# Kernel optimization log

Measured on AMD Instinct MI355X. Metric: run time of the kernel, lower is better.

The kernel has to match this reference:

```python
import jax, jax.numpy as jnp
import numpy as np
import math

E = 8          # num_experts
IN = 1024      # input_size
HID = 512      # head_size (expert hidden)
TOP_K = 2
B, P = 8, 1024


def setup_inputs() -> dict:
    key = jax.random.key(0)
    k1, k2, k3, k4, k5 = jax.random.split(key, 5)
    # expert weights init like ParallelExperts.reset_parameters (uniform xavier-ish)
    std1 = math.sqrt(2.0 / (IN + HID)); a1 = math.sqrt(3.0) * std1
    std2 = math.sqrt(2.0 / (HID + IN)); a2 = math.sqrt(3.0) * std2
    return {
        "x": jax.random.normal(k1, (B, P, IN), dtype=jnp.float32),
        "Q_isp": jax.random.normal(k2, (B, P, 1, IN), dtype=jnp.float32),
        "K_isp": jax.random.normal(k3, (B, P, E, IN), dtype=jnp.float32),
        "w1": jax.random.uniform(k4, (E, IN, HID), minval=-a1, maxval=a1, dtype=jnp.float32),
        "w2": jax.random.uniform(k5, (E, HID, IN), minval=-a2, maxval=a2, dtype=jnp.float32),
    }


def _gates(Q_isp, K_isp):
    # attention-based gating, eval path (no noise)
    N = K_isp.shape[2]
    scale = 1.0 / math.sqrt(K_isp.shape[-1])
    # [B,P,1,N] -> [T,N]
    scores = jnp.einsum('bpqd,bpnd->bpqn', Q_isp, K_isp)[:, :, 0, :].reshape(-1, N) * scale
    logits = jnp.nan_to_num(scores, nan=0.0, posinf=20.0, neginf=-20.0)
    probs = jax.nn.softmax(logits, axis=1)
    top_g, top_i = jax.lax.top_k(probs, TOP_K)
    # renormalize top-k gates; denominator detached as in torch (.detach())
    top_g = top_g / jax.lax.stop_gradient(top_g.sum(axis=1, keepdims=True) + 1e-6)
    T = probs.shape[0]
    gates = jnp.zeros_like(probs).at[jnp.arange(T)[:, None], top_i].set(top_g)
    return gates  # [T, E]


def reference(x, Q_isp, K_isp, w1, w2):
    gates = _gates(Q_isp, K_isp)                       # [T,E]
    T = gates.shape[0]
    xt = x.reshape(T, -1)                              # [T,IN]
    # grouped expert GEMMs (dense-masked form; gates are 0 off top-k)
    h = jax.nn.gelu(jnp.einsum('ti,eio->teo', xt, w1), approximate=False)  # [T,E,HID]
    y = jnp.einsum('teo,eoi->tei', h, w2)              # [T,E,IN]
    out = jnp.einsum('tei,te->ti', y, gates)           # combine with gates
    return out.reshape(x.shape)
```

## Files before the change

### kernel.cpp

```cpp
#include <hip/hip_runtime.h>
#include <math.h>

#define TT 8192
#define NE 8
#define DIN 1024
#define DH 512
#define MT_MAX 136

typedef __attribute__((ext_vector_type(8))) short short8;
typedef __attribute__((ext_vector_type(4))) float f32x4;
typedef __attribute__((ext_vector_type(4))) unsigned short us4;

static const size_t NSLOT      = (size_t)(2 * TT + NE * 128);
static const size_t OFF_BASE   = 0;
static const size_t OFF_TOKEXP = 256;
static const size_t OFF_GPAIR  = OFF_TOKEXP + (size_t)TT * 8;
static const size_t OFF_SLOT0  = OFF_GPAIR  + (size_t)TT * 8;
static const size_t OFF_SLOT1  = OFF_SLOT0  + (size_t)TT * 4;
static const size_t OFF_TOK    = OFF_SLOT1  + (size_t)TT * 4;
static const size_t OFF_GATE   = OFF_TOK    + NSLOT * 4;
static const size_t OFF_XB     = OFF_GATE   + NSLOT * 4;
static const size_t OFF_W1T    = OFF_XB     + (size_t)TT * DIN * 2;
static const size_t OFF_W2T    = OFF_W1T    + (size_t)NE * DH * DIN * 2;
static const size_t OFF_H      = OFF_W2T    + (size_t)NE * DIN * DH * 2;
static const size_t OFF_Y      = OFF_H      + NSLOT * DH * 2;

__device__ __forceinline__ unsigned short f2bf(float f) {
    union { float f; unsigned u; } v; v.f = f;
    unsigned r = (v.u + 0x7fffu + ((v.u >> 16) & 1u)) >> 16;
    return (unsigned short)r;
}
__device__ __forceinline__ float bf2f(unsigned short u) {
    union { unsigned u; float f; } v; v.u = ((unsigned)u) << 16;
    return v.f;
}
__device__ __forceinline__ void async_copy16(const void* g, void* l) {
    __builtin_amdgcn_global_load_lds(
        (const __attribute__((address_space(1))) void*)g,
        (__attribute__((address_space(3))) void*)l, 16, 0, 0);
}

__device__ __forceinline__ float gelu_erf(float u) {
    float z  = 0.70710678118f * u;
    float az = fabsf(z);
    float t  = __builtin_amdgcn_rcpf(__builtin_fmaf(0.3275911f, az, 1.0f));
    float p  = t * (0.254829592f + t * (-0.284496736f + t * (1.421413741f +
               t * (-1.453152027f + t * 1.061405429f))));
    float e2 = exp2f(-1.4426950408889634f * az * az);
    float er = __builtin_fmaf(-p, e2, 1.0f);
    er = copysignf(er, z);
    return 0.5f * u * (1.0f + er);
}

__global__ __launch_bounds__(256) void prep_kernel(
    const float* __restrict__ x, const float* __restrict__ w1, const float* __restrict__ w2,
    const float* __restrict__ Q, const float* __restrict__ Kc,
    unsigned short* __restrict__ xb, unsigned short* __restrict__ w1t,
    unsigned short* __restrict__ w2t,
    int2* __restrict__ tokexp, float2* __restrict__ gpair)
{
    __shared__ float tile[32][33];
    int bid = blockIdx.x;
    int tid = threadIdx.x;

    if (bid < 2048) {
        int wave = tid >> 6, lane = tid & 63;
        int t = bid * 4 + wave;
        const float4* q4 = reinterpret_cast<const float4*>(Q + (size_t)t * DIN);
        const float4* k4 = reinterpret_cast<const float4*>(Kc + (size_t)t * NE * DIN);
        float4 q[4];
#pragma unroll
        for (int j = 0; j < 4; ++j) q[j] = q4[j * 64 + lane];
        float part[NE];
#pragma unroll
        for (int e = 0; e < NE; ++e) {
            float s = 0.0f;
#pragma unroll
            for (int j = 0; j < 4; ++j) {
                float4 kv = k4[e * 256 + j * 64 + lane];
                s += q[j].x * kv.x + q[j].y * kv.y + q[j].z * kv.z + q[j].w * kv.w;
            }
            part[e] = s;
        }
#pragma unroll
        for (int e = 0; e < NE; ++e) {
#pragma unroll
            for (int m = 1; m < 64; m <<= 1) part[e] += __shfl_xor(part[e], m);
        }
        if (lane == 0) {
            float s[NE];
#pragma unroll
            for (int e = 0; e < NE; ++e) {
                float v = part[e] * 0.03125f;
                if (isnan(v)) v = 0.0f;
                else if (isinf(v)) v = (v > 0.0f) ? 20.0f : -20.0f;
                s[e] = v;
            }
            float m = s[0];
            for (int e = 1; e < NE; ++e) m = fmaxf(m, s[e]);
            float p[NE]; float sum = 0.0f;
            for (int e = 0; e < NE; ++e) { p[e] = expf(s[e] - m); sum += p[e]; }
            float inv = 1.0f / sum;
            for (int e = 0; e < NE; ++e) p[e] *= inv;
            int i0 = 0;
            for (int e = 1; e < NE; ++e) if (p[e] > p[i0]) i0 = e;
            int i1 = (i0 == 0) ? 1 : 0;
            for (int e = 0; e < NE; ++e) if (e != i0 && p[e] > p[i1]) i1 = e;
            float denom = p[i0] + p[i1] + 1e-6f;
            tokexp[t] = make_int2(i0, i1);
            gpair[t]  = make_float2(p[i0] / denom, p[i1] / denom);
        }
    } else if (bid < 6144) {
        size_t i = ((size_t)(bid - 2048) * 256 + tid) * 8;
        float4 a = *reinterpret_cast<const float4*>(x + i);
        float4 b = *reinterpret_cast<const float4*>(x + i + 4);
        us4 o0 = { f2bf(a.x), f2bf(a.y), f2bf(a.z), f2bf(a.w) };
        us4 o1 = { f2bf(b.x), f2bf(b.y), f2bf(b.z), f2bf(b.w) };
        *reinterpret_cast<us4*>(xb + i)     = o0;
        *reinterpret_cast<us4*>(xb + i + 4) = o1;
    } else {
        const float* src; unsigned short* dst; int K, N, e, k0, n0;
        if (bid < 10240) {
            int r = bid - 6144; e = r >> 9; int rem = r & 511;
            k0 = (rem & 31) * 32; n0 = (rem >> 5) * 32;
            src = w1; dst = w1t; K = DIN; N = DH;
        } else {
            int r = bid - 10240; e = r >> 9; int rem = r & 511;
            k0 = (rem & 15) * 32; n0 = (rem >> 4) * 32;
            src = w2; dst = w2t; K = DH; N = DIN;
        }
        int tx = tid & 31, ty = tid >> 5;
        const float* s = src + ((size_t)e * K + k0) * N + n0;
#pragma unroll
        for (int r2 = 0; r2 < 32; r2 += 8) tile[ty + r2][tx] = s[(size_t)(ty + r2) * N + tx];
        __syncthreads();
        unsigned short* d = dst + ((size_t)e * N + n0) * K + k0;
#pragma unroll
        for (int r2 = 0; r2 < 32; r2 += 8) d[(size_t)(ty + r2) * K + tx] = f2bf(tile[tx][ty + r2]);
    }
}

__global__ __launch_bounds__(1024) void route_kernel(
    const int2* __restrict__ tokexp, const float2* __restrict__ gpair,
    int* __restrict__ base,
    int* __restrict__ tok_list, float* __restrict__ gate_list,
    int* __restrict__ slot0, int* __restrict__ slot1)
{
    int e = blockIdx.x;
    int tid = threadIdx.x;
    int wave = tid >> 6, lane = tid & 63;
    __shared__ int hist[NE];
    __shared__ int wsum[16];
    __shared__ int running;

    if (tid < NE) hist[tid] = 0;
    __syncthreads();

    int lc[NE];
#pragma unroll
    for (int j = 0; j < NE; ++j) lc[j] = 0;
#pragma unroll
    for (int r = 0; r < TT / 1024; ++r) {
        int2 te = tokexp[r * 1024 + tid];
#pragma unroll
        for (int j = 0; j < NE; ++j) lc[j] += (te.x == j ? 1 : 0) + (te.y == j ? 1 : 0);
    }
#pragma unroll
    for (int j = 0; j < NE; ++j) {
        int v = lc[j];
#pragma unroll
        for (int m = 1; m < 64; m <<= 1) v += __shfl_xor(v, m);
        if (lane == 0) atomicAdd(&hist[j], v);
    }
    __syncthreads();

    int basep[NE + 1];
    basep[0] = 0;
#pragma unroll
    for (int j = 0; j < NE; ++j) basep[j + 1] = basep[j] + ((hist[j] + 127) & ~127);

    if (tid == 0) {
        base[e] = basep[e];
        if (e == 0) base[NE] = basep[NE];
        running = basep[e];
    }
    __syncthreads();

    int myb = basep[e];
    int cnt_e = hist[e];
#pragma unroll 1
    for (int r = 0; r < TT / 1024; ++r) {
        int t = r * 1024 + tid;
        int2 te = tokexp[t];
        float2 g = gpair[t];
        bool f0 = (te.x == e), f1 = (te.y == e);
        bool f = f0 || f1;
        unsigned long long mask = __ballot(f);
        int mypos = __popcll(mask & ((1ull << lane) - 1ull));
        if (lane == 0) wsum[wave] = __popcll(mask);
        __syncthreads();
        int off = 0, total = 0;
        for (int w = 0; w < 16; ++w) {
            int c = wsum[w];
            if (w < wave) off += c;
            total += c;
        }
        int pos = running + off + mypos;
        if (f) {
            tok_list[pos]  = t;
            gate_list[pos] = f0 ? g.x : g.y;
            if (f0) slot0[t] = pos; else slot1[t] = pos;
        }
        __syncthreads();
        if (tid == 0) running += total;
        __syncthreads();
    }

    int padn = ((cnt_e + 127) & ~127) - cnt_e;
    if (tid < padn) {
        tok_list[myb + cnt_e + tid]  = 0;
        gate_list[myb + cnt_e + tid] = 0.0f;
    }
}

__global__ __launch_bounds__(256) void gemm1_kernel(
    const unsigned short* __restrict__ xb, const unsigned short* __restrict__ w1t,
    const int* __restrict__ base,
    const int* __restrict__ tok_list, unsigned short* __restrict__ h)
{
    int bv[NE + 1];
#pragma unroll
    for (int i = 0; i <= NE; ++i) bv[i] = base[i];
    int g0 = blockIdx.x * 128;
    if (g0 >= bv[NE]) return;
    int e = 0;
#pragma unroll
    for (int i = 1; i < NE; ++i) if (g0 >= bv[i]) e = i;

    int n0 = blockIdx.y * 128;

    __shared__ __align__(16) char smem[65536];

    int tid = threadIdx.x;
    int w = tid >> 6, lane = tid & 63;
    int wm = w & 1, wn = w >> 1;
    int mcol = lane & 15;
    int kq = (lane >> 4) * 8;

    int ra0 = tok_list[g0 + (2 * w + 0) * 16 + mcol];
    int ra1 = tok_list[g0 + (2 * w + 1) * 16 + mcol];

    const unsigned short* w1e = w1t + (size_t)e * DH * DIN;
    const unsigned short* pa0 = xb + (size_t)ra0 * DIN + kq;
    const unsigned short* pa1 = xb + (size_t)ra1 * DIN + kq;
    const unsigned short* pb0 = w1e + (size_t)(n0 + (2 * w + 0) * 16 + mcol) * DIN + kq;
    const unsigned short* pb1 = w1e + (size_t)(n0 + (2 * w + 1) * 16 + mcol) * DIN + kq;

    int d0 = (2 * w + 0) * 1024;
    int d1 = (2 * w + 1) * 1024;

#define STAGE1(buf, koff) do { \
    async_copy16(pa0 + (koff),      (buf) + d0); \
    async_copy16(pa1 + (koff),      (buf) + d1); \
    async_copy16(pa0 + (koff) + 32, (buf) + 8192  + d0); \
    async_copy16(pa1 + (koff) + 32, (buf) + 8192  + d1); \
    async_copy16(pb0 + (koff),      (buf) + 16384 + d0); \
    async_copy16(pb1 + (koff),      (buf) + 16384 + d1); \
    async_copy16(pb0 + (koff) + 32, (buf) + 24576 + d0); \
    async_copy16(pb1 + (koff) + 32, (buf) + 24576 + d1); \
} while (0)

    f32x4 acc[4][4];
#pragma unroll
    for (int i = 0; i < 4; i++)
#pragma unroll
        for (int j = 0; j < 4; j++) acc[i][j] = {0.f, 0.f, 0.f, 0.f};

    char* cur = smem;
    char* nxt = smem + 32768;

    STAGE1(cur, 0);
    __syncthreads();

    const int NT = DIN / 64;
    for (int t = 0; t < NT; ++t) {
        if (t + 1 < NT) STAGE1(nxt, (t + 1) * 64);
#pragma unroll
        for (int half = 0; half < 2; ++half) {
            const char* cb = cur + half * 8192;
            short8 af[4], bfr[4];
#pragma unroll
            for (int mt = 0; mt < 4; ++mt)
                af[mt] = *reinterpret_cast<const short8*>(cb + (wm * 4 + mt) * 1024 + lane * 16);
#pragma unroll
            for (int nt = 0; nt < 4; ++nt)
                bfr[nt] = *reinterpret_cast<const short8*>(cb + 16384 + (wn * 4 + nt) * 1024 + lane * 16);
#pragma unroll
            for (int mt = 0; mt < 4; ++mt)
#pragma unroll
                for (int nt = 0; nt < 4; ++nt)
                    acc[mt][nt] = __builtin_amdgcn_mfma_f32_16x16x32_bf16(af[mt], bfr[nt], acc[mt][nt], 0, 0, 0);
        }
        __syncthreads();
        char* tmp = cur; cur = nxt; nxt = tmp;
    }
#undef STAGE1

#pragma unroll
    for (int mt = 0; mt < 4; ++mt) {
        int rbase = (wm * 4 + mt) * 16 + ((lane >> 4) * 4);
#pragma unroll
        for (int r = 0; r < 4; ++r) {
            int row = rbase + r;
#pragma unroll
            for (int nt = 0; nt < 4; ++nt) {
                float g = gelu_erf(acc[mt][nt][r]);
                int col = n0 + (wn * 4 + nt) * 16 + mcol;
                h[(size_t)(g0 + row) * DH + col] = f2bf(g);
            }
        }
    }
}

__global__ __launch_bounds__(256) void gemm2_kernel(
    const unsigned short* __restrict__ h, const unsigned short* __restrict__ w2t,
    const int* __restrict__ base,
    const float* __restrict__ gate_list, unsigned short* __restrict__ y)
{
    int bv[NE + 1];
#pragma unroll
    for (int i = 0; i <= NE; ++i) bv[i] = base[i];
    int g0 = blockIdx.x * 128;
    if (g0 >= bv[NE]) return;
    int e = 0;
#pragma unroll
    for (int i = 1; i < NE; ++i) if (g0 >= bv[i]) e = i;

    int n0 = blockIdx.y * 128;

    __shared__ __align__(16) char smem[65536];

    int tid = threadIdx.x;
    int w = tid >> 6, lane = tid & 63;
    int wm = w & 1, wn = w >> 1;
    int mcol = lane & 15;
    int kq = (lane >> 4) * 8;

    const unsigned short* w2e = w2t + (size_t)e * DIN * DH;
    const unsigned short* pa0 = h + (size_t)(g0 + (2 * w + 0) * 16 + mcol) * DH + kq;
    const unsigned short* pa1 = h + (size_t)(g0 + (2 * w + 1) * 16 + mcol) * DH + kq;
    const unsigned short* pb0 = w2e + (size_t)(n0 + (2 * w + 0) * 16 + mcol) * DH + kq;
    const unsigned short* pb1 = w2e + (size_t)(n0 + (2 * w + 1) * 16 + mcol) * DH + kq;

    int d0 = (2 * w + 0) * 1024;
    int d1 = (2 * w + 1) * 1024;

#define STAGE2(buf, koff) do { \
    async_copy16(pa0 + (koff),      (buf) + d0); \
    async_copy16(pa1 + (koff),      (buf) + d1); \
    async_copy16(pa0 + (koff) + 32, (buf) + 8192  + d0); \
    async_copy16(pa1 + (koff) + 32, (buf) + 8192  + d1); \
    async_copy16(pb0 + (koff),      (buf) + 16384 + d0); \
    async_copy16(pb1 + (koff),      (buf) + 16384 + d1); \
    async_copy16(pb0 + (koff) + 32, (buf) + 24576 + d0); \
    async_copy16(pb1 + (koff) + 32, (buf) + 24576 + d1); \
} while (0)

    f32x4 acc[4][4];
#pragma unroll
    for (int i = 0; i < 4; i++)
#pragma unroll
        for (int j = 0; j < 4; j++) acc[i][j] = {0.f, 0.f, 0.f, 0.f};

    char* cur = smem;
    char* nxt = smem + 32768;

    STAGE2(cur, 0);
    __syncthreads();

    const int NT = DH / 64;
    for (int t = 0; t < NT; ++t) {
        if (t + 1 < NT) STAGE2(nxt, (t + 1) * 64);
#pragma unroll
        for (int half = 0; half < 2; ++half) {
            const char* cb = cur + half * 8192;
            short8 af[4], bfr[4];
#pragma unroll
            for (int mt = 0; mt < 4; ++mt)
                af[mt] = *reinterpret_cast<const short8*>(cb + (wm * 4 + mt) * 1024 + lane * 16);
#pragma unroll
            for (int nt = 0; nt < 4; ++nt)
                bfr[nt] = *reinterpret_cast<const short8*>(cb + 16384 + (wn * 4 + nt) * 1024 + lane * 16);
#pragma unroll
            for (int mt = 0; mt < 4; ++mt)
#pragma unroll
                for (int nt = 0; nt < 4; ++nt)
                    acc[mt][nt] = __builtin_amdgcn_mfma_f32_16x16x32_bf16(af[mt], bfr[nt], acc[mt][nt], 0, 0, 0);
        }
        __syncthreads();
        char* tmp = cur; cur = nxt; nxt = tmp;
    }
#undef STAGE2

#pragma unroll
    for (int mt = 0; mt < 4; ++mt) {
        int rbase = (wm * 4 + mt) * 16 + ((lane >> 4) * 4);
#pragma unroll
        for (int r = 0; r < 4; ++r) {
            int row = rbase + r;
            float g = gate_list[g0 + row];
#pragma unroll
            for (int nt = 0; nt < 4; ++nt) {
                int col = n0 + (wn * 4 + nt) * 16 + mcol;
                y[(size_t)(g0 + row) * DIN + col] = f2bf(acc[mt][nt][r] * g);
            }
        }
    }
}

__global__ __launch_bounds__(256) void combine_kernel(
    const unsigned short* __restrict__ y,
    const int* __restrict__ slot0, const int* __restrict__ slot1,
    float* __restrict__ out)
{
    int c = threadIdx.x * 4;
#pragma unroll
    for (int r = 0; r < 4; ++r) {
        int t = blockIdx.x * 4 + r;
        const unsigned short* y0 = y + (size_t)slot0[t] * DIN + c;
        const unsigned short* y1 = y + (size_t)slot1[t] * DIN + c;
        us4 u0 = *reinterpret_cast<const us4*>(y0);
        us4 u1 = *reinterpret_cast<const us4*>(y1);
        float4 o;
        o.x = bf2f(u0.x) + bf2f(u1.x);
        o.y = bf2f(u0.y) + bf2f(u1.y);
        o.z = bf2f(u0.z) + bf2f(u1.z);
        o.w = bf2f(u0.w) + bf2f(u1.w);
        *reinterpret_cast<float4*>(out + (size_t)t * DIN + c) = o;
    }
}

extern "C" void kernel_launch(void* const* d_in, const int* in_sizes, int n_in,
                              void* d_out, int out_size, void* d_ws, size_t ws_size,
                              hipStream_t stream) {
    const float* x  = (const float*)d_in[0];
    const float* Q  = (const float*)d_in[1];
    const float* K  = (const float*)d_in[2];
    const float* w1 = (const float*)d_in[3];
    const float* w2 = (const float*)d_in[4];
    float* out = (float*)d_out;

    char* ws = (char*)d_ws;
    int*    base      = (int*)(ws + OFF_BASE);
    int2*   tokexp    = (int2*)(ws + OFF_TOKEXP);
    float2* gpair     = (float2*)(ws + OFF_GPAIR);
    int*    slot0     = (int*)(ws + OFF_SLOT0);
    int*    slot1     = (int*)(ws + OFF_SLOT1);
    int*    tok_list  = (int*)(ws + OFF_TOK);
    float*  gate_list = (float*)(ws + OFF_GATE);
    unsigned short* xb  = (unsigned short*)(ws + OFF_XB);
    unsigned short* w1t = (unsigned short*)(ws + OFF_W1T);
    unsigned short* w2t = (unsigned short*)(ws + OFF_W2T);
    unsigned short* h   = (unsigned short*)(ws + OFF_H);
    unsigned short* y   = (unsigned short*)(ws + OFF_Y);

    prep_kernel<<<14336, 256, 0, stream>>>(x, w1, w2, Q, K, xb, w1t, w2t, tokexp, gpair);
    route_kernel<<<NE, 1024, 0, stream>>>(tokexp, gpair, base, tok_list, gate_list, slot0, slot1);
    gemm1_kernel<<<dim3(MT_MAX, DH / 128), 256, 0, stream>>>(xb, w1t, base, tok_list, h);
    gemm2_kernel<<<dim3(MT_MAX, DIN / 128), 256, 0, stream>>>(h, w2t, base, gate_list, y);
    combine_kernel<<<TT / 4, 256, 0, stream>>>(y, slot0, slot1, out);
}
```

Baseline: 551.5 us.

## Replace double-buffered K loop with 4-slot, 3-deep async copy pipeline

Both expert GEMM kernels now stage K-slices of 32 instead of 64 into a four-slot LDS ring. Three stages are prefetched ahead, and the loop waits on exact vmcnt counts before a single barrier per iteration. The goal is to hide more global-load latency and drop the trailing per-iteration syncthreads. In exchange the kernels run twice as many loop iterations, and correctness now depends on the hand-counted vmcnt values matching the four copies issued per stage.

```diff
diff --git a/kernel.cpp b/kernel.cpp
--- a/kernel.cpp
+++ b/kernel.cpp
@@ -260,14 +260,10 @@
     int d1 = (2 * w + 1) * 1024;
 
 #define STAGE1(buf, koff) do { \
-    async_copy16(pa0 + (koff),      (buf) + d0); \
-    async_copy16(pa1 + (koff),      (buf) + d1); \
-    async_copy16(pa0 + (koff) + 32, (buf) + 8192  + d0); \
-    async_copy16(pa1 + (koff) + 32, (buf) + 8192  + d1); \
-    async_copy16(pb0 + (koff),      (buf) + 16384 + d0); \
-    async_copy16(pb1 + (koff),      (buf) + 16384 + d1); \
-    async_copy16(pb0 + (koff) + 32, (buf) + 24576 + d0); \
-    async_copy16(pb1 + (koff) + 32, (buf) + 24576 + d1); \
+    async_copy16(pa0 + (koff), (buf) + d0); \
+    async_copy16(pa1 + (koff), (buf) + d1); \
+    async_copy16(pb0 + (koff), (buf) + 8192 + d0); \
+    async_copy16(pb1 + (koff), (buf) + 8192 + d1); \
 } while (0)
 
     f32x4 acc[4][4];
@@ -276,33 +272,34 @@
 #pragma unroll
         for (int j = 0; j < 4; j++) acc[i][j] = {0.f, 0.f, 0.f, 0.f};
 
-    char* cur = smem;
-    char* nxt = smem + 32768;
-
-    STAGE1(cur, 0);
-    __syncthreads();
-
-    const int NT = DIN / 64;
+    STAGE1(smem + 0 * 16384, 0);
+    STAGE1(smem + 1 * 16384, 32);
+    STAGE1(smem + 2 * 16384, 64);
+
+    const int NT = DIN / 32;
     for (int t = 0; t < NT; ++t) {
-        if (t + 1 < NT) STAGE1(nxt, (t + 1) * 64);
-#pragma unroll
-        for (int half = 0; half < 2; ++half) {
-            const char* cb = cur + half * 8192;
-            short8 af[4], bfr[4];
-#pragma unroll
-            for (int mt = 0; mt < 4; ++mt)
-                af[mt] = *reinterpret_cast<const short8*>(cb + (wm * 4 + mt) * 1024 + lane * 16);
+        if (t < NT - 2)       asm volatile("s_waitcnt vmcnt(8)" ::: "memory");
+        else if (t == NT - 2) asm volatile("s_waitcnt vmcnt(4)" ::: "memory");
+        else                  asm volatile("s_waitcnt vmcnt(0)" ::: "memory");
+        __builtin_amdgcn_sched_barrier(0);
+        __builtin_amdgcn_s_barrier();
+        __builtin_amdgcn_sched_barrier(0);
+        if (t + 3 < NT) STAGE1(smem + ((t + 3) & 3) * 16384, (t + 3) * 32);
+
+        const char* cb = smem + (t & 3) * 16384;
+        short8 af[4], bfr[4];
+#pragma unroll
+        for (int mt = 0; mt < 4; ++mt)
+            af[mt] = *reinterpret_cast<const short8*>(cb + (wm * 4 + mt) * 1024 + lane * 16);
+#pragma unroll
+        for (int nt = 0; nt < 4; ++nt)
+            bfr[nt] = *reinterpret_cast<const short8*>(cb + 8192 + (wn * 4 + nt) * 1024 + lane * 16);
+#pragma unroll
+        for (int mt = 0; mt < 4; ++mt)
 #pragma unroll
             for (int nt = 0; nt < 4; ++nt)
-                bfr[nt] = *reinterpret_cast<const short8*>(cb + 16384 + (wn * 4 + nt) * 1024 + lane * 16);
-#pragma unroll
-            for (int mt = 0; mt < 4; ++mt)
-#pragma unroll
-                for (int nt = 0; nt < 4; ++nt)
-                    acc[mt][nt] = __builtin_amdgcn_mfma_f32_16x16x32_bf16(af[mt], bfr[nt], acc[mt][nt], 0, 0, 0);
-        }
-        __syncthreads();
-        char* tmp = cur; cur = nxt; nxt = tmp;
+                acc[mt][nt] = __builtin_amdgcn_mfma_f32_16x16x32_bf16(af[mt], bfr[nt], acc[mt][nt], 0, 0, 0);
+        __builtin_amdgcn_sched_barrier(0);
     }
 #undef STAGE1
 
@@ -356,14 +353,10 @@
     int d1 = (2 * w + 1) * 1024;
 
 #define STAGE2(buf, koff) do { \
-    async_copy16(pa0 + (koff),      (buf) + d0); \
-    async_copy16(pa1 + (koff),      (buf) + d1); \
-    async_copy16(pa0 + (koff) + 32, (buf) + 8192  + d0); \
-    async_copy16(pa1 + (koff) + 32, (buf) + 8192  + d1); \
-    async_copy16(pb0 + (koff),      (buf) + 16384 + d0); \
-    async_copy16(pb1 + (koff),      (buf) + 16384 + d1); \
-    async_copy16(pb0 + (koff) + 32, (buf) + 24576 + d0); \
-    async_copy16(pb1 + (koff) + 32, (buf) + 24576 + d1); \
+    async_copy16(pa0 + (koff), (buf) + d0); \
+    async_copy16(pa1 + (koff), (buf) + d1); \
+    async_copy16(pb0 + (koff), (buf) + 8192 + d0); \
+    async_copy16(pb1 + (koff), (buf) + 8192 + d1); \
 } while (0)
 
     f32x4 acc[4][4];
@@ -372,33 +365,34 @@
 #pragma unroll
         for (int j = 0; j < 4; j++) acc[i][j] = {0.f, 0.f, 0.f, 0.f};
 
-    char* cur = smem;
-    char* nxt = smem + 32768;
-
-    STAGE2(cur, 0);
-    __syncthreads();
-
-    const int NT = DH / 64;
+    STAGE2(smem + 0 * 16384, 0);
+    STAGE2(smem + 1 * 16384, 32);
+    STAGE2(smem + 2 * 16384, 64);
+
+    const int NT = DH / 32;
     for (int t = 0; t < NT; ++t) {
-        if (t + 1 < NT) STAGE2(nxt, (t + 1) * 64);
-#pragma unroll
-        for (int half = 0; half < 2; ++half) {
-            const char* cb = cur + half * 8192;
-            short8 af[4], bfr[4];
-#pragma unroll
-            for (int mt = 0; mt < 4; ++mt)
-                af[mt] = *reinterpret_cast<const short8*>(cb + (wm * 4 + mt) * 1024 + lane * 16);
+        if (t < NT - 2)       asm volatile("s_waitcnt vmcnt(8)" ::: "memory");
+        else if (t == NT - 2) asm volatile("s_waitcnt vmcnt(4)" ::: "memory");
+        else                  asm volatile("s_waitcnt vmcnt(0)" ::: "memory");
+        __builtin_amdgcn_sched_barrier(0);
+        __builtin_amdgcn_s_barrier();
+        __builtin_amdgcn_sched_barrier(0);
+        if (t + 3 < NT) STAGE2(smem + ((t + 3) & 3) * 16384, (t + 3) * 32);
+
+        const char* cb = smem + (t & 3) * 16384;
+        short8 af[4], bfr[4];
+#pragma unroll
+        for (int mt = 0; mt < 4; ++mt)
+            af[mt] = *reinterpret_cast<const short8*>(cb + (wm * 4 + mt) * 1024 + lane * 16);
+#pragma unroll
+        for (int nt = 0; nt < 4; ++nt)
+            bfr[nt] = *reinterpret_cast<const short8*>(cb + 8192 + (wn * 4 + nt) * 1024 + lane * 16);
+#pragma unroll
+        for (int mt = 0; mt < 4; ++mt)
 #pragma unroll
             for (int nt = 0; nt < 4; ++nt)
-                bfr[nt] = *reinterpret_cast<const short8*>(cb + 16384 + (wn * 4 + nt) * 1024 + lane * 16);
-#pragma unroll
-            for (int mt = 0; mt < 4; ++mt)
-#pragma unroll
-                for (int nt = 0; nt < 4; ++nt)
-                    acc[mt][nt] = __builtin_amdgcn_mfma_f32_16x16x32_bf16(af[mt], bfr[nt], acc[mt][nt], 0, 0, 0);
-        }
-        __syncthreads();
-        char* tmp = cur; cur = nxt; nxt = tmp;
+                acc[mt][nt] = __builtin_amdgcn_mfma_f32_16x16x32_bf16(af[mt], bfr[nt], acc[mt][nt], 0, 0, 0);
+        __builtin_amdgcn_sched_barrier(0);
     }
 #undef STAGE2
 
```

New measurement: 541.1 us. About the same (-1.9%).
